# Optimization experiments

Measured on AMD Instinct MI355X. Metric: run time of the kernel, lower is better.

The kernel has to match this reference:

```python
import jax, jax.numpy as jnp
import numpy as np

T, B, D_IN, R, D_OUT = 256, 64, 512, 2048, 128
SPARSITY, BETA, THRESH = 0.8, 0.9, 1.0


def setup_inputs() -> dict:
    key = jax.random.key(0)
    ks = jax.random.split(key, 6)
    lim_rec = float(np.sqrt(3.0 / R))  # VarianceScaling(1.0,'fan_avg','uniform') with fan_in=fan_out=R
    return {
        "x_seq": jax.random.normal(ks[0], (T, B, D_IN), jnp.float32),
        "w_in": jax.random.normal(ks[1], (D_IN, R), jnp.float32) / np.sqrt(D_IN).astype(np.float32),
        "b_in": jnp.zeros((R,), jnp.float32),
        "w_rec": jax.random.uniform(ks[2], (R, R), jnp.float32, -lim_rec, lim_rec),
        "w_head": jax.random.normal(ks[3], (R, D_OUT), jnp.float32) / np.sqrt(R).astype(np.float32),
        "b_head": jnp.zeros((D_OUT,), jnp.float32),
    }


def reference(x_seq, w_in, b_in, w_rec, w_head, b_head):
    n = R * R
    keep = max(1, int(n * (1.0 - SPARSITY)))
    scores = jnp.abs(w_rec).reshape(-1)
    thresh = jnp.sort(scores)[n - keep]  # k-th largest of |w_rec| (same threshold as top_k)
    mask = (jnp.abs(w_rec) >= thresh).astype(w_rec.dtype)
    w_eff = w_rec * mask

    # input projection is time-parallel; hoist it out of the scan
    drive_in = jnp.einsum('tbd,dr->tbr', x_seq, w_in) + b_in  # [T,B,R]

    def step(carry, drive_t):
        V, prev_s = carry
        cur = drive_t + prev_s @ w_eff          # sparse recurrent drive
        V = BETA * V + cur                      # LIF integrate (leak + input)
        s = (V > THRESH).astype(x_seq.dtype)    # heaviside spike
        V = V - s * THRESH                      # soft reset
        logits = s @ w_head + b_head
        return (V, s), (logits, jnp.mean(s))

    init = (jnp.zeros((B, R), x_seq.dtype), jnp.zeros((B, R), x_seq.dtype))
    _, (logits_seq, sr_seq) = jax.lax.scan(step, init, drive_in)

    readout = jnp.mean(logits_seq, axis=0)  # readout mode 'mean'
    spike_rate = jnp.asarray([jnp.mean(sr_seq)])
    active_ratio = jnp.mean(mask)
    return readout, logits_seq, spike_rate, active_ratio
```

## Files before the change

### kernel.cpp

```cpp
#include <hip/hip_runtime.h>
#include <hip/hip_bf16.h>
#include <stdint.h>

#define TT 256
#define BB 64
#define DIN 512
#define RR 2048
#define DOUT 128
#define NTOT (RR*RR)
#define NKEEP 838860
#define BETA 0.9f
#define VTH 1.0f


#define FLAG_STRIDE 16

__global__ void k_init(uint32_t* __restrict__ p, int n) {
    int i = blockIdx.x * blockDim.x + threadIdx.x;
    int stride = gridDim.x * blockDim.x;
    for (; i < n; i += stride) p[i] = 0u;
}

__global__ void k_hist(const float* __restrict__ w_rec, uint32_t* __restrict__ hist,
                       const uint32_t* __restrict__ state, int p) {
    __shared__ uint32_t lh[256];
    lh[threadIdx.x] = 0u;
    __syncthreads();
    uint32_t prefix = (p > 0) ? state[0] : 0u;
    int sh = 24 - 8 * p;
    int i = blockIdx.x * 256 + threadIdx.x;
    int stride = gridDim.x * 256;
    for (; i < NTOT; i += stride) {
        uint32_t u = __float_as_uint(fabsf(w_rec[i]));
        bool ok = (p == 0) || ((u >> (sh + 8)) == prefix);
        if (ok) atomicAdd(&lh[(u >> sh) & 255u], 1u);
    }
    __syncthreads();
    uint32_t v = lh[threadIdx.x];
    if (v) atomicAdd(&hist[threadIdx.x], v);
}

__global__ void k_select(uint32_t* __restrict__ hist, uint32_t* __restrict__ state, int p) {
    __shared__ uint32_t lh[256];
    int tid = threadIdx.x;
    lh[tid] = hist[tid];
    hist[tid] = 0u;
    __syncthreads();
    if (tid == 0) {
        uint32_t remaining = (p == 0) ? (uint32_t)NKEEP : state[1];
        int bin = 255;
        for (; bin > 0; --bin) {
            uint32_t c = lh[bin];
            if (c >= remaining) break;
            remaining -= c;
        }
        uint32_t pref = (p == 0) ? 0u : state[0];
        pref = (pref << 8) | (uint32_t)bin;
        state[0] = pref;
        state[1] = remaining;
        if (p == 3) state[2] = pref;
    }
}

__global__ void k_maskcount(float* __restrict__ w, const uint32_t* __restrict__ state,
                            uint32_t* __restrict__ cnts) {
    uint32_t th = state[2];
    uint32_t c = 0;
    int i = blockIdx.x * blockDim.x + threadIdx.x;
    int stride = gridDim.x * blockDim.x;
    for (; i < NTOT / 4; i += stride) {
        float4 v = *(float4*)&w[i * 4];
        if ((__float_as_uint(v.x) & 0x7fffffffu) >= th) c++; else v.x = 0.0f;
        if ((__float_as_uint(v.y) & 0x7fffffffu) >= th) c++; else v.y = 0.0f;
        if ((__float_as_uint(v.z) & 0x7fffffffu) >= th) c++; else v.z = 0.0f;
        if ((__float_as_uint(v.w) & 0x7fffffffu) >= th) c++; else v.w = 0.0f;
        *(float4*)&w[i * 4] = v;
    }
    for (int off = 32; off > 0; off >>= 1) c += __shfl_down(c, off);
    if ((threadIdx.x & 63) == 0 && c) atomicAdd(&cnts[1], c);
}

__global__ __launch_bounds__(256) void k_drive(const float* __restrict__ x,
                                               const float* __restrict__ w_in,
                                               const float* __restrict__ b_in,
                                               float* __restrict__ drive) {
    __shared__ float As[8][128];
    __shared__ float Bs[8][128];
    const int m0 = blockIdx.x * 128;
    const int n0 = blockIdx.y * 128;
    const int tid = threadIdx.x;
    const int tx = tid & 15, ty = tid >> 4;
    const int ar = tid >> 1;
    const int ak = (tid & 1) * 4;
    const int bk = tid >> 5;
    const int bc = (tid & 31) * 4;
    float acc[8][8];
    #pragma unroll
    for (int i = 0; i < 8; ++i)
        #pragma unroll
        for (int j = 0; j < 8; ++j) acc[i][j] = 0.0f;

    for (int k0 = 0; k0 < DIN; k0 += 8) {
        float4 av = *(const float4*)&x[(m0 + ar) * DIN + k0 + ak];
        float4 bv = *(const float4*)&w_in[(size_t)(k0 + bk) * RR + n0 + bc];
        __syncthreads();
        As[ak + 0][ar] = av.x; As[ak + 1][ar] = av.y;
        As[ak + 2][ar] = av.z; As[ak + 3][ar] = av.w;
        *(float4*)&Bs[bk][bc] = bv;
        __syncthreads();
        #pragma unroll
        for (int kk = 0; kk < 8; ++kk) {
            float a[8], b[8];
            *(float4*)&a[0] = *(const float4*)&As[kk][ty * 8];
            *(float4*)&a[4] = *(const float4*)&As[kk][ty * 8 + 4];
            *(float4*)&b[0] = *(const float4*)&Bs[kk][tx * 8];
            *(float4*)&b[4] = *(const float4*)&Bs[kk][tx * 8 + 4];
            #pragma unroll
            for (int i = 0; i < 8; ++i)
                #pragma unroll
                for (int j = 0; j < 8; ++j)
                    acc[i][j] = fmaf(a[i], b[j], acc[i][j]);
        }
    }
    float bb[8];
    #pragma unroll
    for (int j = 0; j < 8; ++j) bb[j] = b_in[n0 + tx * 8 + j];
    #pragma unroll
    for (int i = 0; i < 8; ++i) {
        size_t row = (size_t)(m0 + ty * 8 + i) * RR + n0 + tx * 8;
        float4 v0, v1;
        v0.x = acc[i][0] + bb[0]; v0.y = acc[i][1] + bb[1];
        v0.z = acc[i][2] + bb[2]; v0.w = acc[i][3] + bb[3];
        v1.x = acc[i][4] + bb[4]; v1.y = acc[i][5] + bb[5];
        v1.z = acc[i][6] + bb[6]; v1.w = acc[i][7] + bb[7];
        *(float4*)&drive[row] = v0;
        *(float4*)&drive[row + 4] = v1;
    }
}

__global__ __launch_bounds__(256, 2) void k_scan(const float* __restrict__ w_rec,
                                                 const float* __restrict__ drive,
                                                 uint32_t* mask, unsigned long long* flags,
                                                 uint32_t* cnts) {
    __shared__ __align__(16) int s_list[RR];
    __shared__ int s_n;
    __shared__ uint32_t s_red[4];

    const int tid = threadIdx.x;
    const int blk = blockIdx.x;
    const int cg = blk & 7;
    const int b = blk >> 3;
    const int col = (cg << 8) + tid;
    const int w = tid >> 6;
    const int lane = tid & 63;
    const char* Wp = (const char*)(w_rec + col);

    float V = 0.f;
    uint32_t scnt = 0;
    float dv = drive[(size_t)b * RR + col];

    for (int t = 0; t < TT; ++t) {
        float a = dv;
        if (t > 0) {
            if (tid == 0) {
                const unsigned long long* fl =
                    &flags[(size_t)((t - 1) * BB + b) * FLAG_STRIDE];
                while (__hip_atomic_load(fl, __ATOMIC_RELAXED, __HIP_MEMORY_SCOPE_AGENT)
                       != ~0ull)
                    __builtin_amdgcn_s_sleep(1);
            }
            __syncthreads();
            if (tid < 64) {
                uint32_t m = __hip_atomic_load(&mask[((size_t)(t - 1) * BB + b) * 64 + tid],
                                               __ATOMIC_RELAXED, __HIP_MEMORY_SCOPE_AGENT);
                int p = __popc(m);
                int off = p;
                #pragma unroll
                for (int d = 1; d < 64; d <<= 1) {
                    int o = __shfl_up(off, d);
                    if (tid >= d) off += o;
                }
                if (tid == 63) s_n = off;
                int e = off - p;
                int base = tid << 5;
                while (m) {
                    int bit = __builtin_ctz(m);
                    m &= m - 1;
                    s_list[e++] = (base + bit) << 13;
                }
            }
            __syncthreads();
            const int n = s_n;
            int i = 0;
            for (; i + 64 <= n; i += 64) {
                float v[64];
                #pragma unroll
                for (int u = 0; u < 64; u += 4) {
                    int4 o = *(const int4*)&s_list[i + u];
                    v[u + 0] = *(const float*)(Wp + o.x);
                    v[u + 1] = *(const float*)(Wp + o.y);
                    v[u + 2] = *(const float*)(Wp + o.z);
                    v[u + 3] = *(const float*)(Wp + o.w);
                }
                __builtin_amdgcn_sched_barrier(0);
                #pragma unroll
                for (int j = 0; j < 64; ++j) a += v[j];
            }
            for (; i + 16 <= n; i += 16) {
                float v[16];
                #pragma unroll
                for (int u = 0; u < 16; u += 4) {
                    int4 o = *(const int4*)&s_list[i + u];
                    v[u + 0] = *(const float*)(Wp + o.x);
                    v[u + 1] = *(const float*)(Wp + o.y);
                    v[u + 2] = *(const float*)(Wp + o.z);
                    v[u + 3] = *(const float*)(Wp + o.w);
                }
                __builtin_amdgcn_sched_barrier(0);
                #pragma unroll
                for (int j = 0; j < 16; ++j) a += v[j];
            }
            for (; i + 4 <= n; i += 4) {
                int4 o = *(const int4*)&s_list[i];
                float v0 = *(const float*)(Wp + o.x);
                float v1 = *(const float*)(Wp + o.y);
                float v2 = *(const float*)(Wp + o.z);
                float v3 = *(const float*)(Wp + o.w);
                a += v0; a += v1; a += v2; a += v3;
            }
            for (; i < n; ++i) a += *(const float*)(Wp + s_list[i]);
        }

        V = BETA * V + a;
        bool sp = V > VTH;
        if (sp) V -= VTH;

        unsigned long long bal = __ballot(sp);
        if (lane == 0) {
            __hip_atomic_store(
                (unsigned long long*)&mask[((size_t)t * BB + b) * 64] + (cg * 4 + w),
                bal, __ATOMIC_RELAXED, __HIP_MEMORY_SCOPE_AGENT);
            scnt += (uint32_t)__popcll(bal);
        }
        __syncthreads();
        if (tid == 0)
            __hip_atomic_store(
                (uint8_t*)&flags[(size_t)(t * BB + b) * FLAG_STRIDE] + cg, (uint8_t)0xFF,
                __ATOMIC_RELEASE, __HIP_MEMORY_SCOPE_AGENT);
        __builtin_amdgcn_sched_barrier(0);
        if (t + 1 < TT)
            dv = drive[((size_t)(t + 1) * BB + b) * RR + col];
    }

    if (lane == 0) s_red[w] = scnt;
    __syncthreads();
    if (tid == 0) {
        uint32_t s = s_red[0] + s_red[1] + s_red[2] + s_red[3];
        if (s) atomicAdd(&cnts[0], s);
    }
}

__global__ __launch_bounds__(128) void k_head(const uint32_t* __restrict__ mask,
                                              const float* __restrict__ w_head,
                                              const float* __restrict__ b_head,
                                              float* __restrict__ logits) {
    __shared__ __align__(16) int s_list[RR];
    __shared__ int s_n;
    int tb = blockIdx.x;
    int tid = threadIdx.x;
    if (tid < 64) {
        uint32_t m = mask[tb * 64 + tid];
        int p = __popc(m);
        int off = p;
        #pragma unroll
        for (int d = 1; d < 64; d <<= 1) {
            int o = __shfl_up(off, d);
            if (tid >= d) off += o;
        }
        if (tid == 63) s_n = off;
        int e = off - p;
        int base = tid << 5;
        while (m) {
            int bit = __builtin_ctz(m);
            m &= m - 1;
            s_list[e++] = (base + bit) << 9;
        }
    }
    __syncthreads();
    const char* Wp = (const char*)(w_head + tid);
    float acc = b_head[tid];
    const int n = s_n;
    int i = 0;
    for (; i + 16 <= n; i += 16) {
        float v[16];
        #pragma unroll
        for (int u = 0; u < 16; u += 4) {
            int4 o = *(const int4*)&s_list[i + u];
            v[u + 0] = *(const float*)(Wp + o.x);
            v[u + 1] = *(const float*)(Wp + o.y);
            v[u + 2] = *(const float*)(Wp + o.z);
            v[u + 3] = *(const float*)(Wp + o.w);
        }
        __builtin_amdgcn_sched_barrier(0);
        #pragma unroll
        for (int j = 0; j < 16; ++j) acc += v[j];
    }
    for (; i < n; ++i) acc += *(const float*)(Wp + s_list[i]);
    logits[(size_t)tb * DOUT + tid] = acc;
}

__global__ __launch_bounds__(128) void k_readout(const float* __restrict__ logits,
                                                 float* __restrict__ readout) {
    int b = blockIdx.x, cidx = threadIdx.x;
    float s = 0.0f;
    for (int t = 0; t < TT; ++t)
        s += logits[(size_t)t * (BB * DOUT) + b * DOUT + cidx];
    readout[b * DOUT + cidx] = s * (1.0f / (float)TT);
}

__global__ void k_scalars(const uint32_t* __restrict__ cnts, float* __restrict__ out) {
    if (threadIdx.x == 0 && blockIdx.x == 0) {
        out[BB * DOUT + TT * BB * DOUT]     = (float)cnts[0] / (float)(TT * BB * RR);
        out[BB * DOUT + TT * BB * DOUT + 1] = (float)cnts[1] / (float)NTOT;
    }
}

extern "C" void kernel_launch(void* const* d_in, const int* in_sizes, int n_in,
                              void* d_out, int out_size, void* d_ws, size_t ws_size,
                              hipStream_t stream) {
    const float* x      = (const float*)d_in[0];
    const float* w_in   = (const float*)d_in[1];
    const float* b_in   = (const float*)d_in[2];
    float*       w_rec  = (float*)d_in[3];
    const float* w_head = (const float*)d_in[4];
    const float* b_head = (const float*)d_in[5];
    float* out = (float*)d_out;

    float*    drive = (float*)d_ws;
    uint32_t* mask  = (uint32_t*)((char*)d_ws + 134217728u);
    unsigned long long* flags = (unsigned long long*)(mask + (TT * BB * 64));
    uint32_t* hist  = (uint32_t*)(flags + (size_t)TT * BB * FLAG_STRIDE);
    uint32_t* state = hist + 256;
    uint32_t* cnts  = state + 8;

    k_init<<<256, 256, 0, stream>>>((uint32_t*)flags,
                                    TT * BB * FLAG_STRIDE * 2 + 256 + 8 + 2);

    for (int p = 0; p < 4; ++p) {
        k_hist<<<1024, 256, 0, stream>>>(w_rec, hist, state, p);
        k_select<<<1, 256, 0, stream>>>(hist, state, p);
    }
    k_maskcount<<<1024, 256, 0, stream>>>(w_rec, state, cnts);

    k_drive<<<dim3(128, 16), 256, 0, stream>>>(x, w_in, b_in, drive);

    k_scan<<<512, 256, 0, stream>>>(w_rec, drive, mask, flags, cnts);

    k_head<<<TT * BB, 128, 0, stream>>>(mask, w_head, b_head, out + BB * DOUT);
    k_readout<<<BB, 128, 0, stream>>>(out + BB * DOUT, out);
    k_scalars<<<1, 64, 0, stream>>>(cnts, out);
}
```

Before: 4.280 ms.

## Stream sparse recurrent weight gathers through LDS with a multi-chunk DMA pipeline

Replaces the register-staged gather of recurrent weight rows (selected by the spike list) with direct global-to-LDS loads (global_load_lds), keeping up to three 16-row chunks in flight per wave while earlier chunks are read back from LDS and accumulated. The aim is to hide gather latency in the serial per-timestep scan and to relieve register pressure from the 64-wide unrolled loads. It adds 64 KB of LDS staging per block, which may reduce occupancy below the two blocks per CU the launch bounds assume, and it relies on hand-written waitcnt and asm ordering.

```diff
diff --git a/kernel.cpp b/kernel.cpp
--- a/kernel.cpp
+++ b/kernel.cpp
@@ -138,11 +138,43 @@
     }
 }
 
+__device__ __forceinline__ void dma4(const void* g, void* l) {
+    __builtin_amdgcn_global_load_lds(
+        (const __attribute__((address_space(1))) uint32_t*)(uintptr_t)g,
+        (__attribute__((address_space(3))) uint32_t*)(uintptr_t)l,
+        4, 0, 0);
+}
+
+#define WAITV(n) do { asm volatile("s_waitcnt vmcnt(" #n ")"); \
+                      __builtin_amdgcn_sched_barrier(0); } while (0)
+
+#define ISSUE_CHUNK(cc) do { \
+    const int i0_ = (cc) << 4; \
+    uint32_t sla_ = slbase + ((uint32_t)i0_ << 2); \
+    int4 q0_, q1_, q2_, q3_; \
+    asm volatile("ds_read_b128 %0, %1"           : "=v"(q0_) : "v"(sla_)); \
+    asm volatile("ds_read_b128 %0, %1 offset:16" : "=v"(q1_) : "v"(sla_)); \
+    asm volatile("ds_read_b128 %0, %1 offset:32" : "=v"(q2_) : "v"(sla_)); \
+    asm volatile("ds_read_b128 %0, %1 offset:48" : "=v"(q3_) : "v"(sla_)); \
+    asm volatile("s_waitcnt lgkmcnt(0)"); \
+    __builtin_amdgcn_sched_barrier(0); \
+    float* dst_ = stgen + ((((cc) & 3)) << 10); \
+    dma4(Wpc + q0_.x, dst_      );  dma4(Wpc + q0_.y, dst_ +  64); \
+    dma4(Wpc + q0_.z, dst_ + 128);  dma4(Wpc + q0_.w, dst_ + 192); \
+    dma4(Wpc + q1_.x, dst_ + 256);  dma4(Wpc + q1_.y, dst_ + 320); \
+    dma4(Wpc + q1_.z, dst_ + 384);  dma4(Wpc + q1_.w, dst_ + 448); \
+    dma4(Wpc + q2_.x, dst_ + 512);  dma4(Wpc + q2_.y, dst_ + 576); \
+    dma4(Wpc + q2_.z, dst_ + 640);  dma4(Wpc + q2_.w, dst_ + 704); \
+    dma4(Wpc + q3_.x, dst_ + 768);  dma4(Wpc + q3_.y, dst_ + 832); \
+    dma4(Wpc + q3_.z, dst_ + 896);  dma4(Wpc + q3_.w, dst_ + 960); \
+} while (0)
+
 __global__ __launch_bounds__(256, 2) void k_scan(const float* __restrict__ w_rec,
                                                  const float* __restrict__ drive,
                                                  uint32_t* mask, unsigned long long* flags,
                                                  uint32_t* cnts) {
     __shared__ __align__(16) int s_list[RR];
+    __shared__ __align__(16) float stage[4][4][16][64];
     __shared__ int s_n;
     __shared__ uint32_t s_red[4];
 
@@ -153,7 +185,11 @@
     const int col = (cg << 8) + tid;
     const int w = tid >> 6;
     const int lane = tid & 63;
-    const char* Wp = (const char*)(w_rec + col);
+    const char* Wpc = (const char*)(w_rec + col);
+
+    const uint32_t slbase = (uint32_t)(uintptr_t)&s_list[0];
+    float* const stgen = &stage[w][0][0][0];
+    const uint32_t stbase = (uint32_t)(uintptr_t)stgen + ((uint32_t)lane << 2);
 
     float V = 0.f;
     uint32_t scnt = 0;
@@ -192,43 +228,53 @@
             __syncthreads();
             const int n = s_n;
             int i = 0;
-            for (; i + 64 <= n; i += 64) {
-                float v[64];
-                #pragma unroll
-                for (int u = 0; u < 64; u += 4) {
-                    int4 o = *(const int4*)&s_list[i + u];
-                    v[u + 0] = *(const float*)(Wp + o.x);
-                    v[u + 1] = *(const float*)(Wp + o.y);
-                    v[u + 2] = *(const float*)(Wp + o.z);
-                    v[u + 3] = *(const float*)(Wp + o.w);
+            const int nch = n >> 4;
+            if (nch > 0) {
+                const int pre = nch < 3 ? nch : 3;
+                for (int c = 0; c < pre; ++c) ISSUE_CHUNK(c);
+                for (int c = 0; c < nch; ++c) {
+                    const int rem = nch - 1 - c;
+                    if (rem >= 2)      WAITV(32);
+                    else if (rem == 1) WAITV(16);
+                    else               WAITV(0);
+                    if (c + 3 < nch) ISSUE_CHUNK(c + 3);
+                    uint32_t ca_ = stbase + ((uint32_t)(c & 3) << 12);
+                    float vv0, vv1, vv2, vv3, vv4, vv5, vv6, vv7;
+                    float vv8, vv9, vv10, vv11, vv12, vv13, vv14, vv15;
+                    asm volatile("ds_read_b32 %0, %1"             : "=v"(vv0)  : "v"(ca_));
+                    asm volatile("ds_read_b32 %0, %1 offset:256"  : "=v"(vv1)  : "v"(ca_));
+                    asm volatile("ds_read_b32 %0, %1 offset:512"  : "=v"(vv2)  : "v"(ca_));
+                    asm volatile("ds_read_b32 %0, %1 offset:768"  : "=v"(vv3)  : "v"(ca_));
+                    asm volatile("ds_read_b32 %0, %1 offset:1024" : "=v"(vv4)  : "v"(ca_));
+                    asm volatile("ds_read_b32 %0, %1 offset:1280" : "=v"(vv5)  : "v"(ca_));
+                    asm volatile("ds_read_b32 %0, %1 offset:1536" : "=v"(vv6)  : "v"(ca_));
+                    asm volatile("ds_read_b32 %0, %1 offset:1792" : "=v"(vv7)  : "v"(ca_));
+                    asm volatile("ds_read_b32 %0, %1 offset:2048" : "=v"(vv8)  : "v"(ca_));
+                    asm volatile("ds_read_b32 %0, %1 offset:2304" : "=v"(vv9)  : "v"(ca_));
+                    asm volatile("ds_read_b32 %0, %1 offset:2560" : "=v"(vv10) : "v"(ca_));
+                    asm volatile("ds_read_b32 %0, %1 offset:2816" : "=v"(vv11) : "v"(ca_));
+                    asm volatile("ds_read_b32 %0, %1 offset:3072" : "=v"(vv12) : "v"(ca_));
+                    asm volatile("ds_read_b32 %0, %1 offset:3328" : "=v"(vv13) : "v"(ca_));
+                    asm volatile("ds_read_b32 %0, %1 offset:3584" : "=v"(vv14) : "v"(ca_));
+                    asm volatile("ds_read_b32 %0, %1 offset:3840" : "=v"(vv15) : "v"(ca_));
+                    asm volatile("s_waitcnt lgkmcnt(0)");
+                    __builtin_amdgcn_sched_barrier(0);
+                    a += vv0;  a += vv1;  a += vv2;  a += vv3;
+                    a += vv4;  a += vv5;  a += vv6;  a += vv7;
+                    a += vv8;  a += vv9;  a += vv10; a += vv11;
+                    a += vv12; a += vv13; a += vv14; a += vv15;
                 }
-                __builtin_amdgcn_sched_barrier(0);
-                #pragma unroll
-                for (int j = 0; j < 64; ++j) a += v[j];
-            }
-            for (; i + 16 <= n; i += 16) {
-                float v[16];
-                #pragma unroll
-                for (int u = 0; u < 16; u += 4) {
-                    int4 o = *(const int4*)&s_list[i + u];
-                    v[u + 0] = *(const float*)(Wp + o.x);
-                    v[u + 1] = *(const float*)(Wp + o.y);
-                    v[u + 2] = *(const float*)(Wp + o.z);
-                    v[u + 3] = *(const float*)(Wp + o.w);
-                }
-                __builtin_amdgcn_sched_barrier(0);
-                #pragma unroll
-                for (int j = 0; j < 16; ++j) a += v[j];
+                i = nch << 4;
             }
             for (; i + 4 <= n; i += 4) {
                 int4 o = *(const int4*)&s_list[i];
-                float v0 = *(const float*)(Wp + o.x);
-                float v1 = *(const float*)(Wp + o.y);
-                float v2 = *(const float*)(Wp + o.z);
-                float v3 = *(const float*)(Wp + o.w);
+                float v0 = *(const float*)(Wpc + o.x);
+                float v1 = *(const float*)(Wpc + o.y);
+                float v2 = *(const float*)(Wpc + o.z);
+                float v3 = *(const float*)(Wpc + o.w);
                 a += v0; a += v1; a += v2; a += v3;
             }
-            for (; i < n; ++i) a += *(const float*)(Wp + s_list[i]);
+            for (; i < n; ++i) a += *(const float*)(Wpc + s_list[i]);
         }
 
         V = BETA * V + a;
```

Measured after the change: 4.433 ms. 1.04x slower.

## Scan over precompiled per-column sparse weight lists, two batches per block

Applied to the files above, without the earlier changes.

Adds a preprocessing kernel that packs the nonzero masked recurrent weights of each column into a coalesced, column-compressed list of (value, row) pairs, capped at a fixed maximum per column. The scan kernel no longer builds a spike index list and gathers from the dense matrix. Each thread walks its column's nonzero list, tests each row's spike bit from shared memory and accumulates for two batch rows at once, so every weight load is shared between two batches. This trades spike-proportional gathers for a fixed nonzero-proportional coalesced stream, and halves the grid. The CSC build runs on only 8 serial blocks, which may be slow. The per-column cap can silently drop weights if a column exceeds it.

```diff
diff --git a/kernel.cpp b/kernel.cpp
--- a/kernel.cpp
+++ b/kernel.cpp
@@ -11,9 +11,11 @@
 #define NKEEP 838860
 #define BETA 0.9f
 #define VTH 1.0f
+#define KMAX 576
 
 
 #define FLAG_STRIDE 16
+#define ENT_OFF 140513280u
 
 __global__ void k_init(uint32_t* __restrict__ p, int n) {
     int i = blockIdx.x * blockDim.x + threadIdx.x;
@@ -78,6 +80,28 @@
     }
     for (int off = 32; off > 0; off >>= 1) c += __shfl_down(c, off);
     if ((threadIdx.x & 63) == 0 && c) atomicAdd(&cnts[1], c);
+}
+
+__global__ __launch_bounds__(256) void k_csc(const float* __restrict__ w,
+                                             uint32_t* __restrict__ ent,
+                                             uint32_t* __restrict__ cnt) {
+    const int cg = blockIdx.x;
+    const int tid = threadIdx.x;
+    const float* wp = w + (cg << 8) + tid;
+    uint32_t* ebase = ent + (size_t)cg * KMAX * 512 + tid * 2;
+    int c = 0;
+    for (int row = 0; row < RR; ++row) {
+        uint32_t vb = __float_as_uint(wp[(size_t)row * RR]);
+        if (vb & 0x7fffffffu) {
+            if (c < KMAX) {
+                uint32_t* e = ebase + (size_t)c * 512;
+                e[0] = vb;
+                e[1] = (uint32_t)row;
+            }
+            c++;
+        }
+    }
+    cnt[(cg << 8) + tid] = (uint32_t)(c < KMAX ? c : KMAX);
 }
 
 __global__ __launch_bounds__(256) void k_drive(const float* __restrict__ x,
@@ -138,118 +162,106 @@
     }
 }
 
-__global__ __launch_bounds__(256, 2) void k_scan(const float* __restrict__ w_rec,
-                                                 const float* __restrict__ drive,
-                                                 uint32_t* mask, unsigned long long* flags,
-                                                 uint32_t* cnts) {
-    __shared__ __align__(16) int s_list[RR];
-    __shared__ int s_n;
+__global__ __launch_bounds__(256) void k_scan(const uint32_t* __restrict__ ent,
+                                              const uint32_t* __restrict__ cnt,
+                                              const float* __restrict__ drive,
+                                              uint32_t* mask, unsigned long long* flags,
+                                              uint32_t* cnts) {
+    __shared__ uint32_t umask[64][2];
     __shared__ uint32_t s_red[4];
 
     const int tid = threadIdx.x;
     const int blk = blockIdx.x;
     const int cg = blk & 7;
-    const int b = blk >> 3;
+    const int bg = blk >> 3;
+    const int b0 = bg * 2, b1 = b0 + 1;
     const int col = (cg << 8) + tid;
     const int w = tid >> 6;
     const int lane = tid & 63;
-    const char* Wp = (const char*)(w_rec + col);
-
-    float V = 0.f;
+
+    const uint32_t myn = cnt[col];
+    const uint2* ep = (const uint2*)(ent + (size_t)cg * KMAX * 512) + tid;
+
+    float V0 = 0.f, V1 = 0.f;
     uint32_t scnt = 0;
-    float dv = drive[(size_t)b * RR + col];
+    float dv0 = drive[(size_t)b0 * RR + col];
+    float dv1 = drive[(size_t)b1 * RR + col];
 
     for (int t = 0; t < TT; ++t) {
-        float a = dv;
+        float a0 = dv0, a1 = dv1;
         if (t > 0) {
-            if (tid == 0) {
+            if (tid < 2) {
                 const unsigned long long* fl =
-                    &flags[(size_t)((t - 1) * BB + b) * FLAG_STRIDE];
+                    &flags[(size_t)((t - 1) * BB + b0 + tid) * FLAG_STRIDE];
                 while (__hip_atomic_load(fl, __ATOMIC_RELAXED, __HIP_MEMORY_SCOPE_AGENT)
                        != ~0ull)
                     __builtin_amdgcn_s_sleep(1);
             }
             __syncthreads();
             if (tid < 64) {
-                uint32_t m = __hip_atomic_load(&mask[((size_t)(t - 1) * BB + b) * 64 + tid],
-                                               __ATOMIC_RELAXED, __HIP_MEMORY_SCOPE_AGENT);
-                int p = __popc(m);
-                int off = p;
-                #pragma unroll
-                for (int d = 1; d < 64; d <<= 1) {
-                    int o = __shfl_up(off, d);
-                    if (tid >= d) off += o;
-                }
-                if (tid == 63) s_n = off;
-                int e = off - p;
-                int base = tid << 5;
-                while (m) {
-                    int bit = __builtin_ctz(m);
-                    m &= m - 1;
-                    s_list[e++] = (base + bit) << 13;
-                }
+                uint32_t m0 = __hip_atomic_load(
+                    &mask[((size_t)(t - 1) * BB + b0) * 64 + tid],
+                    __ATOMIC_RELAXED, __HIP_MEMORY_SCOPE_AGENT);
+                uint32_t m1 = __hip_atomic_load(
+                    &mask[((size_t)(t - 1) * BB + b1) * 64 + tid],
+                    __ATOMIC_RELAXED, __HIP_MEMORY_SCOPE_AGENT);
+                umask[tid][0] = m0;
+                umask[tid][1] = m1;
             }
             __syncthreads();
-            const int n = s_n;
-            int i = 0;
-            for (; i + 64 <= n; i += 64) {
-                float v[64];
-                #pragma unroll
-                for (int u = 0; u < 64; u += 4) {
-                    int4 o = *(const int4*)&s_list[i + u];
-                    v[u + 0] = *(const float*)(Wp + o.x);
-                    v[u + 1] = *(const float*)(Wp + o.y);
-                    v[u + 2] = *(const float*)(Wp + o.z);
-                    v[u + 3] = *(const float*)(Wp + o.w);
-                }
-                __builtin_amdgcn_sched_barrier(0);
-                #pragma unroll
-                for (int j = 0; j < 64; ++j) a += v[j];
-            }
-            for (; i + 16 <= n; i += 16) {
-                float v[16];
-                #pragma unroll
-                for (int u = 0; u < 16; u += 4) {
-                    int4 o = *(const int4*)&s_list[i + u];
-                    v[u + 0] = *(const float*)(Wp + o.x);
-                    v[u + 1] = *(const float*)(Wp + o.y);
-                    v[u + 2] = *(const float*)(Wp + o.z);
-                    v[u + 3] = *(const float*)(Wp + o.w);
-                }
-                __builtin_amdgcn_sched_barrier(0);
-                #pragma unroll
-                for (int j = 0; j < 16; ++j) a += v[j];
-            }
-            for (; i + 4 <= n; i += 4) {
-                int4 o = *(const int4*)&s_list[i];
-                float v0 = *(const float*)(Wp + o.x);
-                float v1 = *(const float*)(Wp + o.y);
-                float v2 = *(const float*)(Wp + o.z);
-                float v3 = *(const float*)(Wp + o.w);
-                a += v0; a += v1; a += v2; a += v3;
-            }
-            for (; i < n; ++i) a += *(const float*)(Wp + s_list[i]);
-        }
-
-        V = BETA * V + a;
-        bool sp = V > VTH;
-        if (sp) V -= VTH;
-
-        unsigned long long bal = __ballot(sp);
+
+            #define PROC(e_) { \
+                uint32_t row_ = (e_).y; \
+                uint2 mm_ = *(const uint2*)&umask[row_ >> 5][0]; \
+                uint32_t sh_ = row_ & 31u; \
+                uint32_t s0_ = 0u - ((mm_.x >> sh_) & 1u); \
+                uint32_t s1_ = 0u - ((mm_.y >> sh_) & 1u); \
+                a0 += __uint_as_float((e_).x & s0_); \
+                a1 += __uint_as_float((e_).x & s1_); }
+
+            uint32_t j = 0;
+            for (; j + 4 <= myn; j += 4) {
+                uint2 e0 = ep[(size_t)(j + 0) * 256];
+                uint2 e1 = ep[(size_t)(j + 1) * 256];
+                uint2 e2 = ep[(size_t)(j + 2) * 256];
+                uint2 e3 = ep[(size_t)(j + 3) * 256];
+                PROC(e0) PROC(e1) PROC(e2) PROC(e3)
+            }
+            for (; j < myn; ++j) {
+                uint2 e = ep[(size_t)j * 256];
+                PROC(e)
+            }
+            #undef PROC
+        }
+
+        V0 = BETA * V0 + a0;
+        bool sp0 = V0 > VTH;
+        if (sp0) V0 -= VTH;
+        V1 = BETA * V1 + a1;
+        bool sp1 = V1 > VTH;
+        if (sp1) V1 -= VTH;
+
+        unsigned long long bal0 = __ballot(sp0);
+        unsigned long long bal1 = __ballot(sp1);
         if (lane == 0) {
             __hip_atomic_store(
-                (unsigned long long*)&mask[((size_t)t * BB + b) * 64] + (cg * 4 + w),
-                bal, __ATOMIC_RELAXED, __HIP_MEMORY_SCOPE_AGENT);
-            scnt += (uint32_t)__popcll(bal);
+                (unsigned long long*)&mask[((size_t)t * BB + b0) * 64] + (cg * 4 + w),
+                bal0, __ATOMIC_RELAXED, __HIP_MEMORY_SCOPE_AGENT);
+            __hip_atomic_store(
+                (unsigned long long*)&mask[((size_t)t * BB + b1) * 64] + (cg * 4 + w),
+                bal1, __ATOMIC_RELAXED, __HIP_MEMORY_SCOPE_AGENT);
+            scnt += (uint32_t)__popcll(bal0) + (uint32_t)__popcll(bal1);
         }
         __syncthreads();
-        if (tid == 0)
+        if (tid < 2)
             __hip_atomic_store(
-                (uint8_t*)&flags[(size_t)(t * BB + b) * FLAG_STRIDE] + cg, (uint8_t)0xFF,
-                __ATOMIC_RELEASE, __HIP_MEMORY_SCOPE_AGENT);
+                (uint8_t*)&flags[(size_t)(t * BB + b0 + tid) * FLAG_STRIDE] + cg,
+                (uint8_t)0xFF, __ATOMIC_RELEASE, __HIP_MEMORY_SCOPE_AGENT);
         __builtin_amdgcn_sched_barrier(0);
-        if (t + 1 < TT)
-            dv = drive[((size_t)(t + 1) * BB + b) * RR + col];
+        if (t + 1 < TT) {
+            dv0 = drive[((size_t)(t + 1) * BB + b0) * RR + col];
+            dv1 = drive[((size_t)(t + 1) * BB + b1) * RR + col];
+        }
     }
 
     if (lane == 0) s_red[w] = scnt;
@@ -342,6 +354,8 @@
     uint32_t* hist  = (uint32_t*)(flags + (size_t)TT * BB * FLAG_STRIDE);
     uint32_t* state = hist + 256;
     uint32_t* cnts  = state + 8;
+    uint32_t* ent   = (uint32_t*)((char*)d_ws + ENT_OFF);
+    uint32_t* cntc  = ent + (size_t)8 * KMAX * 512;
 
     k_init<<<256, 256, 0, stream>>>((uint32_t*)flags,
                                     TT * BB * FLAG_STRIDE * 2 + 256 + 8 + 2);
@@ -352,9 +366,11 @@
     }
     k_maskcount<<<1024, 256, 0, stream>>>(w_rec, state, cnts);
 
+    k_csc<<<8, 256, 0, stream>>>(w_rec, ent, cntc);
+
     k_drive<<<dim3(128, 16), 256, 0, stream>>>(x, w_in, b_in, drive);
 
-    k_scan<<<512, 256, 0, stream>>>(w_rec, drive, mask, flags, cnts);
+    k_scan<<<256, 256, 0, stream>>>(ent, cntc, drive, mask, flags, cnts);
 
     k_head<<<TT * BB, 128, 0, stream>>>(mask, w_head, b_head, out + BB * DOUT);
     k_readout<<<BB, 128, 0, stream>>>(out + BB * DOUT, out);
```

Measured after the change: 9.649 ms. +125.5%, slower.
